# Performance work log

Hardware: AMD Instinct MI355X
Metric: run time of the kernel (lower is better)

Reference implementation:

```python
import jax, jax.numpy as jnp
import numpy as np

BN_EPS = 1e-5


def conv1x1(x, w, b):
    # x: [B,C,H,W], w: [O,C], b: [O]
    return jnp.einsum('oc,bchw->bohw', w, x) + b[None, :, None, None]


def setup_inputs() -> dict:
    key = jax.random.key(0)
    ks = jax.random.split(key, 8)
    B, C, H, W = 4, 256, 64, 64
    Ci = C // 2  # inter_channels
    std = 0.01
    return {
        'x': jax.random.normal(ks[0], (B, C, H, W), dtype=jnp.float32),
        'w_g': jax.random.normal(ks[1], (Ci, C), dtype=jnp.float32) * std,
        'b_g': jnp.zeros((Ci,), jnp.float32),
        'w_theta': jax.random.normal(ks[2], (Ci, C), dtype=jnp.float32) * std,
        'b_theta': jnp.zeros((Ci,), jnp.float32),
        'w_phi': jax.random.normal(ks[3], (Ci, C), dtype=jnp.float32) * std,
        'b_phi': jnp.zeros((Ci,), jnp.float32),
        'w_out': jax.random.normal(ks[4], (C, Ci), dtype=jnp.float32) * std,
        'b_out': jnp.zeros((C,), jnp.float32),
        'bn_gamma': jax.random.normal(ks[5], (C,), dtype=jnp.float32),
        'bn_beta': jnp.zeros((C,), jnp.float32),
    }


def reference(x, w_g, b_g, w_theta, b_theta, w_phi, b_phi, w_out, b_out, bn_gamma, bn_beta):
    B, C, H, W = x.shape
    Ci = w_g.shape[0]
    N = H * W
    # 1x1 conv projections -> flatten spatial to tokens
    g_x = conv1x1(x, w_g, b_g).reshape(B, Ci, N)          # [B,Ci,N]
    theta_x = conv1x1(x, w_theta, b_theta).reshape(B, Ci, N)
    phi_x = conv1x1(x, w_phi, b_phi).reshape(B, Ci, N)
    # dense non-causal attention over N=HW tokens (no scaling)
    f = jnp.einsum('bcn,bcm->bnm', theta_x, phi_x)        # [B,N,N]
    f_div_C = jax.nn.softmax(f, axis=-1)
    y = jnp.einsum('bnm,bcm->bcn', f_div_C, g_x)          # [B,Ci,N]
    y = y.reshape(B, Ci, H, W)
    # output 1x1 conv + BatchNorm2d (training mode: batch statistics)
    W_y = conv1x1(y, w_out, b_out)                        # [B,C,H,W]
    mean = W_y.mean(axis=(0, 2, 3))
    var = W_y.var(axis=(0, 2, 3))
    W_y = (W_y - mean[None, :, None, None]) * jax.lax.rsqrt(var + BN_EPS)[None, :, None, None]
    W_y = W_y * bn_gamma[None, :, None, None] + bn_beta[None, :, None, None]
    return W_y + x
```

## Files before the change

### kernel.cpp

```cpp
#include <hip/hip_runtime.h>

#define N_TOK 4096
#define C_IN 256
#define CI_ 128

typedef unsigned short u16;
typedef unsigned int   u32;
typedef __attribute__((ext_vector_type(8))) short bf16x8;
typedef __attribute__((ext_vector_type(4))) float f32x4;

__device__ __forceinline__ float lo16f(u32 u){ union{u32 i; float f;} c; c.i = u << 16; return c.f; }
__device__ __forceinline__ float hi16f(u32 u){ union{u32 i; float f;} c; c.i = u & 0xffff0000u; return c.f; }
__device__ __forceinline__ void bf8f(const uint4 u, float* f){
    f[0]=lo16f(u.x); f[1]=hi16f(u.x); f[2]=lo16f(u.y); f[3]=hi16f(u.y);
    f[4]=lo16f(u.z); f[5]=hi16f(u.z); f[6]=lo16f(u.w); f[7]=hi16f(u.w);
}
__device__ __forceinline__ float bf1f(u16 v){ union{u32 i; float f;} c; c.i = ((u32)v)<<16; return c.f; }
__device__ __forceinline__ u16 f2bf(float f){
    union{float f; u32 i;} c; c.f = f;
    u32 i = c.i;
    u32 r = (i + 0x7fffu + ((i >> 16) & 1u)) >> 16;
    return (u16)r;
}
__device__ __forceinline__ u32 packbf(float a, float b){
    return (u32)f2bf(a) | ((u32)f2bf(b) << 16);
}

__device__ __forceinline__ void load8(const void* base, size_t idx, int flag, float* f){
    if (flag) {
        const float* p = (const float*)base + idx;
        *(float4*)&f[0] = *(const float4*)p;
        *(float4*)&f[4] = *(const float4*)(p + 4);
    } else {
        uint4 u = *(const uint4*)((const u16*)base + idx);
        bf8f(u, f);
    }
}
__device__ __forceinline__ void load4(const void* base, size_t idx, int flag, float* f){
    if (flag) {
        float4 v = *(const float4*)((const float*)base + idx);
        f[0]=v.x; f[1]=v.y; f[2]=v.z; f[3]=v.w;
    } else {
        uint2 u = *(const uint2*)((const u16*)base + idx);
        f[0]=lo16f(u.x); f[1]=hi16f(u.x); f[2]=lo16f(u.y); f[3]=hi16f(u.y);
    }
}

__global__ __launch_bounds__(256) void convert_params_kernel(
    const void* wg, const void* wt, const void* wp, const void* wo,
    const void* bg, const void* bt, const void* bp, const void* bo,
    const void* gm, const void* bt2,
    int* __restrict__ flagp, float* __restrict__ canon, u16* __restrict__ canon_bf,
    float* __restrict__ stats)
{
    __shared__ int sflag;
    const int tid = threadIdx.x;
    if (tid < 64) {
        int cnt = 0;
        const u16* wgp = (const u16*)wg;
        for (int i = tid; i < 256; i += 64) {
            u16 v = wgp[2 * i];
            if (((v >> 7) & 0xFF) >= 128) cnt++;
        }
        #pragma unroll
        for (int off = 32; off; off >>= 1) cnt += __shfl_down(cnt, off);
        if (tid == 0) sflag = (cnt >= 8) ? 1 : 0;
    }
    __syncthreads();
    const int f = sflag;
    if (blockIdx.x == 0 && tid == 0) *flagp = f;

    int idx = blockIdx.x * 256 + tid;
    if (idx >= 132224) {
        int j = idx - 132224;
        if (j < 4096) stats[j] = 0.f;
        return;
    }
    const void* src; int loc;
    if      (idx < 32768)  { src = wg;  loc = idx; }
    else if (idx < 65536)  { src = wt;  loc = idx - 32768; }
    else if (idx < 98304)  { src = wp;  loc = idx - 65536; }
    else if (idx < 131072) { src = wo;  loc = idx - 98304; }
    else if (idx < 131200) { src = bg;  loc = idx - 131072; }
    else if (idx < 131328) { src = bt;  loc = idx - 131200; }
    else if (idx < 131456) { src = bp;  loc = idx - 131328; }
    else if (idx < 131712) { src = bo;  loc = idx - 131456; }
    else if (idx < 131968) { src = gm;  loc = idx - 131712; }
    else                   { src = bt2; loc = idx - 131968; }
    float v = f ? ((const float*)src)[loc] : bf1f(((const u16*)src)[loc]);
    canon[idx] = v;
    if (idx < 131072) canon_bf[idx] = f2bf(v);
}

__global__ __launch_bounds__(512) void proj_kernel(
    const void* __restrict__ x, const float* __restrict__ canon,
    const u16* __restrict__ wbf, const int* __restrict__ flagp,
    u16* __restrict__ gbuf, u16* __restrict__ tbufT, u16* __restrict__ pbufT)
{
    __shared__ __align__(16) u16 plds[64 * 400];
    const int flag = *flagp;
    const int b  = blockIdx.y;
    const int n0 = blockIdx.x * 64;
    const int tid = threadIdx.x;
    const int w    = tid >> 6;
    const int lane = tid & 63;
    const int col  = lane & 15;
    const int quad = lane >> 4;
    const int rw   = w * 48;

    f32x4 acc[3][4];
    #pragma unroll
    for (int i = 0; i < 3; ++i)
        #pragma unroll
        for (int j = 0; j < 4; ++j) acc[i][j] = (f32x4){0.f,0.f,0.f,0.f};

    const size_t xb = (size_t)b * C_IN * N_TOK;
    const int sk  = tid >> 4;
    const int sn4 = (tid & 15) * 4;
    const int skk = sk ^ (((sn4 >> 3) & 3) << 3);

    float pre[4];
    load4(x, xb + (size_t)sk * N_TOK + n0 + sn4, flag, pre);

    for (int kc = 0; kc < 8; ++kc) {
        const int k0 = kc * 32;
        __syncthreads();
        #pragma unroll
        for (int i = 0; i < 4; ++i) plds[(sn4 + i) * 40 + skk] = f2bf(pre[i]);
        __syncthreads();
        if (kc < 7)
            load4(x, xb + (size_t)(k0 + 32 + sk) * N_TOK + n0 + sn4, flag, pre);
        bf16x8 bfr[4];
        #pragma unroll
        for (int nf = 0; nf < 4; ++nf) {
            int n = nf * 16 + col;
            int q2 = quad ^ ((n >> 3) & 3);
            bfr[nf] = *(const bf16x8*)&plds[n * 40 + q2 * 8];
        }
        #pragma unroll
        for (int rs = 0; rs < 3; ++rs) {
            bf16x8 afr = *(const bf16x8*)&wbf[(size_t)(rw + rs * 16 + col) * 256 + k0 + quad * 8];
            #pragma unroll
            for (int nf = 0; nf < 4; ++nf)
                acc[rs][nf] = __builtin_amdgcn_mfma_f32_16x16x32_bf16(afr, bfr[nf], acc[rs][nf], 0, 0, 0);
        }
    }

    __syncthreads();
    #pragma unroll
    for (int rs = 0; rs < 3; ++rs) {
        int r0 = rw + rs * 16 + quad * 4;
        float b0 = canon[131072 + r0 + 0];
        float b1 = canon[131072 + r0 + 1];
        float b2 = canon[131072 + r0 + 2];
        float b3 = canon[131072 + r0 + 3];
        #pragma unroll
        for (int nf = 0; nf < 4; ++nf) {
            int n = nf * 16 + col;
            uint2 pv;
            pv.x = packbf(acc[rs][nf][0] + b0, acc[rs][nf][1] + b1);
            pv.y = packbf(acc[rs][nf][2] + b2, acc[rs][nf][3] + b3);
            *(uint2*)&plds[n * 400 + r0] = pv;
        }
    }
    __syncthreads();

    const size_t bN = (size_t)b * N_TOK;
    {
        int r = tid & 127, nq = tid >> 7;
        u16 tmp[16];
        #pragma unroll
        for (int j = 0; j < 16; ++j) tmp[j] = plds[(nq * 16 + j) * 400 + r];
        u16* dst = &gbuf[((size_t)b * CI_ + r) * N_TOK + n0 + nq * 16];
        *(uint4*)(dst + 0) = *(uint4*)&tmp[0];
        *(uint4*)(dst + 8) = *(uint4*)&tmp[8];
    }
    {
        int n = tid & 63, part = tid >> 6;
        const u16* src = (part < 4) ? &plds[n * 400 + 128 + part * 32]
                                    : &plds[n * 400 + 256 + (part - 4) * 32];
        u16* dst = (part < 4) ? &tbufT[(bN + n0 + n) * CI_ + part * 32]
                              : &pbufT[(bN + n0 + n) * CI_ + (part - 4) * 32];
        #pragma unroll
        for (int v = 0; v < 4; ++v) *(uint4*)(dst + v * 8) = *(const uint4*)(src + v * 8);
    }
}

#define PH_OFF(p) ((p) * 16384)
#define G_OFF(p)  (32768 + (p) * 20480)
#define PB_OFF    73728
#define MST_OFF   90112
#define LST_OFF   90368
#define SMEM_SZ   90624
#define YB_OFF    32768

__global__ __launch_bounds__(512) void attn_kernel(
    const u16* __restrict__ tbufT, const u16* __restrict__ pbufT,
    const u16* __restrict__ gbuf,
    const u16* __restrict__ wbf, const float* __restrict__ canon,
    u16* __restrict__ wyb, float* __restrict__ stats)
{
    __shared__ __align__(16) char smem[SMEM_SZ];
    const int b   = blockIdx.y;
    const int q0  = blockIdx.x * 64;
    const int tid = threadIdx.x;
    const int w    = tid >> 6;
    const int lane = tid & 63;
    const int col  = lane & 15;
    const int quad = lane >> 4;
    const int wq   = w & 3;
    const int ms   = w >> 2;
    const int qw   = wq * 16;

    bf16x8 thf[4];
    {
        const u16* tb = tbufT + ((size_t)b * N_TOK + q0 + qw + col) * CI_;
        #pragma unroll
        for (int kc = 0; kc < 4; ++kc)
            thf[kc] = *(const bf16x8*)(tb + kc * 32 + quad * 8);
    }

    f32x4 yacc[8];
    #pragma unroll
    for (int i = 0; i < 8; ++i) yacc[i] = (f32x4){0.f, 0.f, 0.f, 0.f};
    float m_st = -3.0e38f, l_st = 0.f;

    const size_t bN = (size_t)b * N_TOK;
    const size_t bC = (size_t)b * CI_;

    for (int s = 0; s < 32; ++s) {
        __syncthreads();
        #pragma unroll
        for (int p = 0; p < 2; ++p) {
            const int m0p = (2 * s + p) * 64;
            #pragma unroll
            for (int i = 0; i < 2; ++i) {
                int cid = i * 512 + tid;
                int m = cid >> 4, h = cid & 15;
                uint4 v = *(const uint4*)(pbufT + (bN + m0p + m) * CI_ + h * 8);
                *(uint4*)(smem + PH_OFF(p) + m * 256 + ((h ^ (m & 15)) << 4)) = v;
            }
            #pragma unroll
            for (int i = 0; i < 2; ++i) {
                int cid = i * 512 + tid;
                int c = cid >> 3, h = cid & 7;
                uint4 v = *(const uint4*)(gbuf + (bC + c) * N_TOK + m0p + h * 8);
                *(uint4*)(smem + G_OFF(p) + c * 160 + ((h ^ (c & 7)) << 4)) = v;
            }
        }
        __syncthreads();

        f32x4 sacc[4];
        #pragma unroll
        for (int i = 0; i < 4; ++i) sacc[i] = (f32x4){0.f, 0.f, 0.f, 0.f};
        #pragma unroll
        for (int kc = 0; kc < 4; ++kc) {
            #pragma unroll
            for (int msub = 0; msub < 4; ++msub) {
                int m = msub * 16 + col;
                int h = kc * 4 + quad;
                bf16x8 af = *(const bf16x8*)(smem + PH_OFF(ms) + m * 256 + ((h ^ (m & 15)) << 4));
                sacc[msub] = __builtin_amdgcn_mfma_f32_16x16x32_bf16(af, thf[kc], sacc[msub], 0, 0, 0);
            }
        }

        float tmax = sacc[0][0];
        #pragma unroll
        for (int i = 0; i < 4; ++i)
            #pragma unroll
            for (int r = 0; r < 4; ++r) tmax = fmaxf(tmax, sacc[i][r]);
        tmax = fmaxf(tmax, __shfl_xor(tmax, 16));
        tmax = fmaxf(tmax, __shfl_xor(tmax, 32));
        float m_new = fmaxf(m_st, tmax);
        float p16[16], ps = 0.f;
        #pragma unroll
        for (int i = 0; i < 4; ++i)
            #pragma unroll
            for (int r = 0; r < 4; ++r) {
                float pv = __expf(sacc[i][r] - m_new);
                p16[i * 4 + r] = pv;
                ps += pv;
            }
        ps += __shfl_xor(ps, 16);
        ps += __shfl_xor(ps, 32);
        float alpha = __expf(m_st - m_new);
        l_st = l_st * alpha + ps;
        m_st = m_new;
        #pragma unroll
        for (int i = 0; i < 8; ++i) {
            yacc[i][0] *= alpha; yacc[i][1] *= alpha;
            yacc[i][2] *= alpha; yacc[i][3] *= alpha;
        }

        {
            char* pb = smem + PB_OFF + w * 2048 + col * 128;
            #pragma unroll
            for (int msub = 0; msub < 4; ++msub) {
                #pragma unroll
                for (int pr = 0; pr < 2; ++pr) {
                    u32 d = packbf(p16[msub * 4 + pr * 2], p16[msub * 4 + pr * 2 + 1]);
                    int h = msub * 2 + (quad >> 1);
                    *(u32*)(pb + ((h ^ (col & 7)) << 4) + (quad & 1) * 8 + pr * 4) = d;
                }
            }
        }
        __asm volatile("s_waitcnt lgkmcnt(0)" ::: "memory");

        bf16x8 pf[2];
        #pragma unroll
        for (int km = 0; km < 2; ++km) {
            int h = km * 4 + quad;
            pf[km] = *(const bf16x8*)(smem + PB_OFF + w * 2048 + col * 128 + ((h ^ (col & 7)) << 4));
        }
        #pragma unroll
        for (int csub = 0; csub < 8; ++csub) {
            #pragma unroll
            for (int km = 0; km < 2; ++km) {
                int c = csub * 16 + col;
                int h = km * 4 + quad;
                bf16x8 gf = *(const bf16x8*)(smem + G_OFF(ms) + c * 160 + ((h ^ (c & 7)) << 4));
                yacc[csub] = __builtin_amdgcn_mfma_f32_16x16x32_bf16(gf, pf[km], yacc[csub], 0, 0, 0);
            }
        }
    }

    __syncthreads();
    if (ms == 1) {
        char* mb = smem + wq * 8192 + col * 512;
        #pragma unroll
        for (int csub = 0; csub < 8; ++csub)
            *(f32x4*)(mb + (((csub * 4 + quad) ^ col) << 4)) = yacc[csub];
        if (quad == 0) {
            *(float*)(smem + MST_OFF + (wq * 16 + col) * 4) = m_st;
            *(float*)(smem + LST_OFF + (wq * 16 + col) * 4) = l_st;
        }
    }
    __syncthreads();
    if (ms == 0) {
        float m1 = *(const float*)(smem + MST_OFF + (wq * 16 + col) * 4);
        float l1 = *(const float*)(smem + LST_OFF + (wq * 16 + col) * 4);
        float M  = fmaxf(m_st, m1);
        float a0 = __expf(m_st - M), a1 = __expf(m1 - M);
        float li = 1.f / (l_st * a0 + l1 * a1);
        float s0 = a0 * li, s1 = a1 * li;
        const char* mb = smem + wq * 8192 + col * 512;
        const int q = qw + col;
        #pragma unroll
        for (int csub = 0; csub < 8; ++csub) {
            f32x4 y1 = *(const f32x4*)(mb + (((csub * 4 + quad) ^ col) << 4));
            uint2 pv;
            pv.x = packbf(yacc[csub][0] * s0 + y1[0] * s1, yacc[csub][1] * s0 + y1[1] * s1);
            pv.y = packbf(yacc[csub][2] * s0 + y1[2] * s1, yacc[csub][3] * s0 + y1[3] * s1);
            int chunk = csub * 2 + (quad >> 1);
            *(uint2*)(smem + YB_OFF + q * 256 + ((chunk ^ (q & 15)) << 4) + (quad & 1) * 8) = pv;
        }
    }
    __syncthreads();

    const u16* wo = wbf + 98304;
    f32x4 oacc[2][4];
    #pragma unroll
    for (int i = 0; i < 2; ++i)
        #pragma unroll
        for (int j = 0; j < 4; ++j) oacc[i][j] = (f32x4){0.f,0.f,0.f,0.f};
    #pragma unroll
    for (int kc = 0; kc < 4; ++kc) {
        bf16x8 bqf[4];
        #pragma unroll
        for (int qf = 0; qf < 4; ++qf) {
            int q = qf * 16 + col;
            int h = kc * 4 + quad;
            bqf[qf] = *(const bf16x8*)(smem + YB_OFF + q * 256 + ((h ^ (q & 15)) << 4));
        }
        #pragma unroll
        for (int os = 0; os < 2; ++os) {
            bf16x8 afr = *(const bf16x8*)&wo[(size_t)(w * 32 + os * 16 + col) * CI_ + kc * 32 + quad * 8];
            #pragma unroll
            for (int qf = 0; qf < 4; ++qf)
                oacc[os][qf] = __builtin_amdgcn_mfma_f32_16x16x32_bf16(afr, bqf[qf], oacc[os][qf], 0, 0, 0);
        }
    }
    const int bucket = (blockIdx.x + blockIdx.y) & 7;
    float* sb = stats + bucket * 512;
    #pragma unroll
    for (int os = 0; os < 2; ++os) {
        int ob = w * 32 + os * 16 + quad * 4;
        #pragma unroll
        for (int i = 0; i < 4; ++i) {
            float bb = canon[131456 + ob + i];
            float s1 = 0.f, s2 = 0.f;
            u16* dst = &wyb[((size_t)b * C_IN + ob + i) * N_TOK + q0 + col];
            #pragma unroll
            for (int qf = 0; qf < 4; ++qf) {
                float v = oacc[os][qf][i] + bb;
                dst[qf * 16] = f2bf(v);
                s1 += v;
                s2 += v * v;
            }
            #pragma unroll
            for (int off = 8; off; off >>= 1) {
                s1 += __shfl_xor(s1, off);
                s2 += __shfl_xor(s2, off);
            }
            if (col == 0) {
                atomicAdd(&sb[ob + i], s1);
                atomicAdd(&sb[256 + ob + i], s2);
            }
        }
    }
}

__global__ __launch_bounds__(256) void bnorm_kernel(
    const u16* __restrict__ wyb, const void* __restrict__ x,
    const float* __restrict__ stats,
    const float* __restrict__ canon, const int* __restrict__ flagp,
    void* __restrict__ outv)
{
    const int flag = *flagp;
    size_t base = ((size_t)blockIdx.x * 256 + threadIdx.x) * 8;
    int o = (int)((base >> 12) & 255);
    float sum1 = 0.f, sum2 = 0.f;
    #pragma unroll
    for (int k = 0; k < 8; ++k) {
        sum1 += stats[k * 512 + o];
        sum2 += stats[k * 512 + 256 + o];
    }
    float mean = sum1 * (1.f / 16384.f);
    float var  = sum2 * (1.f / 16384.f) - mean * mean;
    float r = rsqrtf(var + 1e-5f);
    float gm = canon[131712 + o], bt = canon[131968 + o];
    uint4 wu = *(const uint4*)&wyb[base];
    float wv[8]; bf8f(wu, wv);
    float xf[8]; load8(x, base, flag, xf);
    float ov[8];
    #pragma unroll
    for (int i = 0; i < 8; ++i)
        ov[i] = (wv[i] - mean) * r * gm + bt + xf[i];
    if (flag) {
        float* op = (float*)outv + base;
        *(float4*)op       = *(float4*)&ov[0];
        *(float4*)(op + 4) = *(float4*)&ov[4];
    } else {
        uint4 res;
        res.x = packbf(ov[0], ov[1]);
        res.y = packbf(ov[2], ov[3]);
        res.z = packbf(ov[4], ov[5]);
        res.w = packbf(ov[6], ov[7]);
        *(uint4*)((u16*)outv + base) = res;
    }
}

extern "C" void kernel_launch(void* const* d_in, const int* in_sizes, int n_in,
                              void* d_out, int out_size, void* d_ws, size_t ws_size,
                              hipStream_t stream)
{
    const void* x   = d_in[0];
    const void* w_g = d_in[1];
    const void* b_g = d_in[2];
    const void* w_t = d_in[3];
    const void* b_t = d_in[4];
    const void* w_p = d_in[5];
    const void* b_p = d_in[6];
    const void* w_o = d_in[7];
    const void* b_o = d_in[8];
    const void* gm  = d_in[9];
    const void* bt  = d_in[10];

    char* base = (char*)d_ws;
    float* canon    = (float*)base;
    u16*   canon_bf = (u16*)(base + 528896);
    int*   flagp    = (int*)(base + 791040);
    float* stats    = (float*)(base + 791296);
    u16*   gbuf     = (u16*)(base + 1048576);
    u16*   tbufT    = (u16*)(base + 5242880);
    u16*   pbufT    = (u16*)(base + 9437184);
    u16*   wyb      = (u16*)(base + 13631488);

    convert_params_kernel<<<533, 256, 0, stream>>>(w_g, w_t, w_p, w_o, b_g, b_t, b_p, b_o,
                                                   gm, bt, flagp, canon, canon_bf, stats);
    proj_kernel<<<dim3(64, 4), 512, 0, stream>>>(x, canon, canon_bf, flagp, gbuf, tbufT, pbufT);
    attn_kernel<<<dim3(64, 4), 512, 0, stream>>>(tbufT, pbufT, gbuf, canon_bf, canon, wyb, stats);
    bnorm_kernel<<<2048, 256, 0, stream>>>(wyb, x, stats, canon, flagp, d_out);
}
```

Before: 188.1 us.

## Double-buffer attention K/V tiles via async global-to-LDS loads; pre-transpose x

The attention kernel now streams phi and g tiles straight into a double-buffered LDS region using global_load_lds DMA. The next step's tile is issued while the current one is computed, synchronised with explicit waitcnt and barrier instructions, replacing the register-staged loads and two __syncthreads per step. A new transpose kernel converts x to token-major bf16 so the projection kernel can read MFMA operands straight from global memory without LDS staging. This costs an extra kernel launch, a workspace buffer and a larger LDS footprint (about 148KB), which may limit occupancy.

```diff
diff --git a/kernel.cpp b/kernel.cpp
--- a/kernel.cpp
+++ b/kernel.cpp
@@ -44,6 +44,12 @@
         uint2 u = *(const uint2*)((const u16*)base + idx);
         f[0]=lo16f(u.x); f[1]=hi16f(u.x); f[2]=lo16f(u.y); f[3]=hi16f(u.y);
     }
+}
+
+__device__ __forceinline__ void dma16(const u16* g, char* l){
+    __builtin_amdgcn_global_load_lds(
+        (const __attribute__((address_space(1))) u32*)g,
+        (__attribute__((address_space(3))) u32*)l, 16, 0, 0);
 }
 
 __global__ __launch_bounds__(256) void convert_params_kernel(
@@ -92,13 +98,39 @@
     if (idx < 131072) canon_bf[idx] = f2bf(v);
 }
 
+__global__ __launch_bounds__(256) void xpose_kernel(
+    const void* __restrict__ x, const int* __restrict__ flagp, u16* __restrict__ xbfT)
+{
+    __shared__ u16 t[64][72];
+    const int flag = *flagp;
+    const int b = blockIdx.z, k0 = blockIdx.y * 64, n0 = blockIdx.x * 64;
+    const int tid = threadIdx.x;
+    const size_t xb = (size_t)b * C_IN * N_TOK;
+    {
+        int kk = tid >> 4, n4 = (tid & 15) * 4;
+        #pragma unroll
+        for (int i = 0; i < 4; ++i) {
+            float f[4];
+            load4(x, xb + (size_t)(k0 + kk + i * 16) * N_TOK + n0 + n4, flag, f);
+            #pragma unroll
+            for (int j = 0; j < 4; ++j) t[n4 + j][kk + i * 16] = f2bf(f[j]);
+        }
+    }
+    __syncthreads();
+    {
+        int kq = tid & 3, n = tid >> 2;
+        u16* dst = &xbfT[((size_t)b * N_TOK + n0 + n) * C_IN + k0 + kq * 16];
+        *(uint4*)(dst + 0) = *(const uint4*)&t[n][kq * 16];
+        *(uint4*)(dst + 8) = *(const uint4*)&t[n][kq * 16 + 8];
+    }
+}
+
 __global__ __launch_bounds__(512) void proj_kernel(
-    const void* __restrict__ x, const float* __restrict__ canon,
-    const u16* __restrict__ wbf, const int* __restrict__ flagp,
+    const u16* __restrict__ xbfT, const float* __restrict__ canon,
+    const u16* __restrict__ wbf,
     u16* __restrict__ gbuf, u16* __restrict__ tbufT, u16* __restrict__ pbufT)
 {
     __shared__ __align__(16) u16 plds[64 * 400];
-    const int flag = *flagp;
     const int b  = blockIdx.y;
     const int n0 = blockIdx.x * 64;
     const int tid = threadIdx.x;
@@ -107,6 +139,7 @@
     const int col  = lane & 15;
     const int quad = lane >> 4;
     const int rw   = w * 48;
+    const size_t bN = (size_t)b * N_TOK;
 
     f32x4 acc[3][4];
     #pragma unroll
@@ -114,39 +147,21 @@
         #pragma unroll
         for (int j = 0; j < 4; ++j) acc[i][j] = (f32x4){0.f,0.f,0.f,0.f};
 
-    const size_t xb = (size_t)b * C_IN * N_TOK;
-    const int sk  = tid >> 4;
-    const int sn4 = (tid & 15) * 4;
-    const int skk = sk ^ (((sn4 >> 3) & 3) << 3);
-
-    float pre[4];
-    load4(x, xb + (size_t)sk * N_TOK + n0 + sn4, flag, pre);
-
+    #pragma unroll
     for (int kc = 0; kc < 8; ++kc) {
-        const int k0 = kc * 32;
-        __syncthreads();
-        #pragma unroll
-        for (int i = 0; i < 4; ++i) plds[(sn4 + i) * 40 + skk] = f2bf(pre[i]);
-        __syncthreads();
-        if (kc < 7)
-            load4(x, xb + (size_t)(k0 + 32 + sk) * N_TOK + n0 + sn4, flag, pre);
         bf16x8 bfr[4];
         #pragma unroll
-        for (int nf = 0; nf < 4; ++nf) {
-            int n = nf * 16 + col;
-            int q2 = quad ^ ((n >> 3) & 3);
-            bfr[nf] = *(const bf16x8*)&plds[n * 40 + q2 * 8];
-        }
+        for (int nf = 0; nf < 4; ++nf)
+            bfr[nf] = *(const bf16x8*)&xbfT[(bN + n0 + nf * 16 + col) * C_IN + kc * 32 + quad * 8];
         #pragma unroll
         for (int rs = 0; rs < 3; ++rs) {
-            bf16x8 afr = *(const bf16x8*)&wbf[(size_t)(rw + rs * 16 + col) * 256 + k0 + quad * 8];
+            bf16x8 afr = *(const bf16x8*)&wbf[(size_t)(rw + rs * 16 + col) * 256 + kc * 32 + quad * 8];
             #pragma unroll
             for (int nf = 0; nf < 4; ++nf)
                 acc[rs][nf] = __builtin_amdgcn_mfma_f32_16x16x32_bf16(afr, bfr[nf], acc[rs][nf], 0, 0, 0);
         }
     }
 
-    __syncthreads();
     #pragma unroll
     for (int rs = 0; rs < 3; ++rs) {
         int r0 = rw + rs * 16 + quad * 4;
@@ -165,7 +180,6 @@
     }
     __syncthreads();
 
-    const size_t bN = (size_t)b * N_TOK;
     {
         int r = tid & 127, nq = tid >> 7;
         u16 tmp[16];
@@ -186,13 +200,10 @@
     }
 }
 
-#define PH_OFF(p) ((p) * 16384)
-#define G_OFF(p)  (32768 + (p) * 20480)
-#define PB_OFF    73728
-#define MST_OFF   90112
-#define LST_OFF   90368
-#define SMEM_SZ   90624
-#define YB_OFF    32768
+#define PB2   131072
+#define MST2  147456
+#define LST2  147712
+#define SMEM2 147968
 
 __global__ __launch_bounds__(512) void attn_kernel(
     const u16* __restrict__ tbufT, const u16* __restrict__ pbufT,
@@ -200,7 +211,7 @@
     const u16* __restrict__ wbf, const float* __restrict__ canon,
     u16* __restrict__ wyb, float* __restrict__ stats)
 {
-    __shared__ __align__(16) char smem[SMEM_SZ];
+    __shared__ __align__(16) char smem[SMEM2];
     const int b   = blockIdx.y;
     const int q0  = blockIdx.x * 64;
     const int tid = threadIdx.x;
@@ -211,44 +222,64 @@
     const int wq   = w & 3;
     const int ms   = w >> 2;
     const int qw   = wq * 16;
+    const size_t bN = (size_t)b * N_TOK;
+    const size_t bC = (size_t)b * CI_;
 
     bf16x8 thf[4];
     {
-        const u16* tb = tbufT + ((size_t)b * N_TOK + q0 + qw + col) * CI_;
+        const u16* tb = tbufT + (bN + q0 + qw + col) * CI_;
         #pragma unroll
         for (int kc = 0; kc < 4; ++kc)
             thf[kc] = *(const bf16x8*)(tb + kc * 32 + quad * 8);
     }
 
+    const u16* sb[8];
+    int ldso[8];
+    int sstep;
+    if (w < 4) {
+        int r = lane >> 4, cp = lane & 15;
+        sstep = 128 * CI_;
+        #pragma unroll
+        for (int j = 0; j < 8; ++j) {
+            int seg = w * 8 + j, p = seg >> 4, m0 = (seg & 15) * 4;
+            int m = m0 + r, h = cp ^ (m & 15);
+            sb[j] = pbufT + (bN + p * 64 + m) * CI_ + h * 8;
+            ldso[j] = p * 16384 + m0 * 256;
+        }
+    } else {
+        int r = lane >> 3, cp = lane & 7;
+        sstep = 128;
+        #pragma unroll
+        for (int j = 0; j < 8; ++j) {
+            int seg = (w - 4) * 8 + j, p = seg >> 4, c0 = (seg & 15) * 8;
+            int c = c0 + r, h = cp ^ (c & 7);
+            sb[j] = gbuf + (bC + c) * N_TOK + p * 64 + h * 8;
+            ldso[j] = 65536 + p * 16384 + c0 * 128;
+        }
+    }
+
     f32x4 yacc[8];
     #pragma unroll
     for (int i = 0; i < 8; ++i) yacc[i] = (f32x4){0.f, 0.f, 0.f, 0.f};
     float m_st = -3.0e38f, l_st = 0.f;
 
-    const size_t bN = (size_t)b * N_TOK;
-    const size_t bC = (size_t)b * CI_;
+    #pragma unroll
+    for (int j = 0; j < 8; ++j) dma16(sb[j], smem + ldso[j]);
 
     for (int s = 0; s < 32; ++s) {
-        __syncthreads();
-        #pragma unroll
-        for (int p = 0; p < 2; ++p) {
-            const int m0p = (2 * s + p) * 64;
-            #pragma unroll
-            for (int i = 0; i < 2; ++i) {
-                int cid = i * 512 + tid;
-                int m = cid >> 4, h = cid & 15;
-                uint4 v = *(const uint4*)(pbufT + (bN + m0p + m) * CI_ + h * 8);
-                *(uint4*)(smem + PH_OFF(p) + m * 256 + ((h ^ (m & 15)) << 4)) = v;
-            }
-            #pragma unroll
-            for (int i = 0; i < 2; ++i) {
-                int cid = i * 512 + tid;
-                int c = cid >> 3, h = cid & 7;
-                uint4 v = *(const uint4*)(gbuf + (bC + c) * N_TOK + m0p + h * 8);
-                *(uint4*)(smem + G_OFF(p) + c * 160 + ((h ^ (c & 7)) << 4)) = v;
-            }
-        }
-        __syncthreads();
+        const int bb = (s & 1) << 15;
+        __asm volatile("s_waitcnt lgkmcnt(0)" ::: "memory");
+        __asm volatile("s_barrier" ::: "memory");
+        if (s < 31) {
+            const int nb = ((s + 1) & 1) << 15;
+            const size_t so = (size_t)(s + 1) * sstep;
+            #pragma unroll
+            for (int j = 0; j < 8; ++j) dma16(sb[j] + so, smem + nb + ldso[j]);
+            __asm volatile("s_waitcnt vmcnt(8)" ::: "memory");
+        } else {
+            __asm volatile("s_waitcnt vmcnt(0)" ::: "memory");
+        }
+        __asm volatile("s_barrier" ::: "memory");
 
         f32x4 sacc[4];
         #pragma unroll
@@ -259,7 +290,7 @@
             for (int msub = 0; msub < 4; ++msub) {
                 int m = msub * 16 + col;
                 int h = kc * 4 + quad;
-                bf16x8 af = *(const bf16x8*)(smem + PH_OFF(ms) + m * 256 + ((h ^ (m & 15)) << 4));
+                bf16x8 af = *(const bf16x8*)(smem + bb + ms * 16384 + m * 256 + ((h ^ (m & 15)) << 4));
                 sacc[msub] = __builtin_amdgcn_mfma_f32_16x16x32_bf16(af, thf[kc], sacc[msub], 0, 0, 0);
             }
         }
@@ -293,7 +324,7 @@
         }
 
         {
-            char* pb = smem + PB_OFF + w * 2048 + col * 128;
+            char* pb = smem + PB2 + w * 2048 + col * 128;
             #pragma unroll
             for (int msub = 0; msub < 4; ++msub) {
                 #pragma unroll
@@ -310,7 +341,7 @@
         #pragma unroll
         for (int km = 0; km < 2; ++km) {
             int h = km * 4 + quad;
-            pf[km] = *(const bf16x8*)(smem + PB_OFF + w * 2048 + col * 128 + ((h ^ (col & 7)) << 4));
+            pf[km] = *(const bf16x8*)(smem + PB2 + w * 2048 + col * 128 + ((h ^ (col & 7)) << 4));
         }
         #pragma unroll
         for (int csub = 0; csub < 8; ++csub) {
@@ -318,7 +349,7 @@
             for (int km = 0; km < 2; ++km) {
                 int c = csub * 16 + col;
                 int h = km * 4 + quad;
-                bf16x8 gf = *(const bf16x8*)(smem + G_OFF(ms) + c * 160 + ((h ^ (c & 7)) << 4));
+                bf16x8 gf = *(const bf16x8*)(smem + 65536 + bb + ms * 16384 + c * 128 + ((h ^ (c & 7)) << 4));
                 yacc[csub] = __builtin_amdgcn_mfma_f32_16x16x32_bf16(gf, pf[km], yacc[csub], 0, 0, 0);
             }
         }
@@ -331,14 +362,14 @@
         for (int csub = 0; csub < 8; ++csub)
             *(f32x4*)(mb + (((csub * 4 + quad) ^ col) << 4)) = yacc[csub];
         if (quad == 0) {
-            *(float*)(smem + MST_OFF + (wq * 16 + col) * 4) = m_st;
-            *(float*)(smem + LST_OFF + (wq * 16 + col) * 4) = l_st;
+            *(float*)(smem + MST2 + (wq * 16 + col) * 4) = m_st;
+            *(float*)(smem + LST2 + (wq * 16 + col) * 4) = l_st;
         }
     }
     __syncthreads();
     if (ms == 0) {
-        float m1 = *(const float*)(smem + MST_OFF + (wq * 16 + col) * 4);
-        float l1 = *(const float*)(smem + LST_OFF + (wq * 16 + col) * 4);
+        float m1 = *(const float*)(smem + MST2 + (wq * 16 + col) * 4);
+        float l1 = *(const float*)(smem + LST2 + (wq * 16 + col) * 4);
         float M  = fmaxf(m_st, m1);
         float a0 = __expf(m_st - M), a1 = __expf(m1 - M);
         float li = 1.f / (l_st * a0 + l1 * a1);
@@ -352,7 +383,7 @@
             pv.x = packbf(yacc[csub][0] * s0 + y1[0] * s1, yacc[csub][1] * s0 + y1[1] * s1);
             pv.y = packbf(yacc[csub][2] * s0 + y1[2] * s1, yacc[csub][3] * s0 + y1[3] * s1);
             int chunk = csub * 2 + (quad >> 1);
-            *(uint2*)(smem + YB_OFF + q * 256 + ((chunk ^ (q & 15)) << 4) + (quad & 1) * 8) = pv;
+            *(uint2*)(smem + 32768 + q * 256 + ((chunk ^ (q & 15)) << 4) + (quad & 1) * 8) = pv;
         }
     }
     __syncthreads();
@@ -370,7 +401,7 @@
         for (int qf = 0; qf < 4; ++qf) {
             int q = qf * 16 + col;
             int h = kc * 4 + quad;
-            bqf[qf] = *(const bf16x8*)(smem + YB_OFF + q * 256 + ((h ^ (q & 15)) << 4));
+            bqf[qf] = *(const bf16x8*)(smem + 32768 + q * 256 + ((h ^ (q & 15)) << 4));
         }
         #pragma unroll
         for (int os = 0; os < 2; ++os) {
@@ -381,18 +412,18 @@
         }
     }
     const int bucket = (blockIdx.x + blockIdx.y) & 7;
-    float* sb = stats + bucket * 512;
+    float* sbk = stats + bucket * 512;
     #pragma unroll
     for (int os = 0; os < 2; ++os) {
         int ob = w * 32 + os * 16 + quad * 4;
         #pragma unroll
         for (int i = 0; i < 4; ++i) {
-            float bb = canon[131456 + ob + i];
+            float bb2 = canon[131456 + ob + i];
             float s1 = 0.f, s2 = 0.f;
             u16* dst = &wyb[((size_t)b * C_IN + ob + i) * N_TOK + q0 + col];
             #pragma unroll
             for (int qf = 0; qf < 4; ++qf) {
-                float v = oacc[os][qf][i] + bb;
+                float v = oacc[os][qf][i] + bb2;
                 dst[qf * 16] = f2bf(v);
                 s1 += v;
                 s2 += v * v;
@@ -403,8 +434,8 @@
                 s2 += __shfl_xor(s2, off);
             }
             if (col == 0) {
-                atomicAdd(&sb[ob + i], s1);
-                atomicAdd(&sb[256 + ob + i], s2);
+                atomicAdd(&sbk[ob + i], s1);
+                atomicAdd(&sbk[256 + ob + i], s2);
             }
         }
     }
@@ -475,10 +506,12 @@
     u16*   tbufT    = (u16*)(base + 5242880);
     u16*   pbufT    = (u16*)(base + 9437184);
     u16*   wyb      = (u16*)(base + 13631488);
+    u16*   xbfT     = (u16*)(base + 22020096);
 
     convert_params_kernel<<<533, 256, 0, stream>>>(w_g, w_t, w_p, w_o, b_g, b_t, b_p, b_o,
                                                    gm, bt, flagp, canon, canon_bf, stats);
-    proj_kernel<<<dim3(64, 4), 512, 0, stream>>>(x, canon, canon_bf, flagp, gbuf, tbufT, pbufT);
+    xpose_kernel<<<dim3(64, 4, 4), 256, 0, stream>>>(x, flagp, xbfT);
+    proj_kernel<<<dim3(64, 4), 512, 0, stream>>>(xbfT, canon, canon_bf, gbuf, tbufT, pbufT);
     attn_kernel<<<dim3(64, 4), 512, 0, stream>>>(tbufT, pbufT, gbuf, canon_bf, canon, wyb, stats);
     bnorm_kernel<<<2048, 256, 0, stream>>>(wyb, x, stats, canon, flagp, d_out);
 }
```

Result: no change. 188.0 us (-0.1%).
